# Performance work log

Measured on AMD Instinct MI355X. Metric: run time of the kernel, lower is better.

## Reference

```python
import jax, jax.numpy as jnp
import numpy as np

B, T, D, K = 16, 4096, 512, 256
ALPHA_MIN = 1e-6


def setup_inputs() -> dict:
    key = jax.random.key(0)
    ks = jax.random.split(key, 5)
    x = jax.random.normal(ks[0], (B, T, D), dtype=jnp.float32)
    # s_imag ~ U(-pi, pi) as in reset_parameters
    s_imag = jax.random.uniform(ks[1], (K,), minval=-np.pi, maxval=np.pi, dtype=jnp.float32)
    # s_real_raw = softplus^{-1}(target_alpha - alpha_min), target_alpha ~ U(0.01, 0.2)
    target_alpha = jax.random.uniform(ks[2], (K,), minval=0.01, maxval=0.2, dtype=jnp.float32)
    y = jnp.clip(target_alpha - ALPHA_MIN, 1e-8, None)
    s_real_raw = jnp.log(jnp.expm1(y))
    # projection weight/bias (spectral norm applied inside reference)
    W = jax.random.normal(ks[3], (K, D), dtype=jnp.float32) / np.sqrt(D)
    b = jnp.zeros((K,), dtype=jnp.float32)
    tau_raw = jnp.zeros((), dtype=jnp.float32)
    return {"x": x, "s_real_raw": s_real_raw, "s_imag": s_imag,
            "tau_raw": tau_raw, "W": W, "b": b}


def _spectral_normalize(W):
    # one power iteration from a fixed random u (mirrors torch spectral_norm buffer,
    # n_power_iterations=1, eps=1e-7); u,v are stop-gradiented like torch buffers.
    eps = 1e-7
    u0 = jax.random.normal(jax.random.key(42), (W.shape[0],), dtype=W.dtype)
    u0 = u0 / jnp.maximum(jnp.linalg.norm(u0), eps)
    v = W.T @ u0
    v = v / jnp.maximum(jnp.linalg.norm(v), eps)
    u = W @ v
    u = u / jnp.maximum(jnp.linalg.norm(u), eps)
    u = jax.lax.stop_gradient(u)
    v = jax.lax.stop_gradient(v)
    sigma = u @ (W @ v)
    return W / sigma


def reference(x, s_real_raw, s_imag, tau_raw, W, b):
    Bx, Tx, Dx = x.shape
    k = s_imag.shape[0]
    tau = jax.nn.softplus(tau_raw) + 1e-3
    alpha0 = (jax.nn.softplus(s_real_raw) + ALPHA_MIN) * tau  # [k]
    omega0 = s_imag * tau                                     # [k]
    # dt is None path: uniform normalized time step
    dt = jnp.asarray(1.0 / max(Tx - 1, 1), dtype=x.dtype)
    rho = jnp.exp(-alpha0 * dt)   # [k], time-invariant since dt is constant
    ct = jnp.cos(omega0 * dt)     # [k]
    st = jnp.sin(omega0 * dt)     # [k]
    # spectral-normalized linear drive u_t = W_sn x_t + b  -> [B,T,k]
    u = jnp.einsum('btd,kd->btk', x, _spectral_normalize(W)) + b

    def step(carry, u_t):
        c, s = carry  # each [B,k]
        c_new = rho * (c * ct - s * st) + u_t
        s_new = rho * (c * st + s * ct)
        return (c_new, s_new), (c_new, s_new)

    z0 = (jnp.zeros((Bx, k), x.dtype), jnp.zeros((Bx, k), x.dtype))
    _, (C, S) = jax.lax.scan(step, z0, jnp.swapaxes(u, 0, 1))  # [T,B,k] each
    C = jnp.swapaxes(C, 0, 1)
    S = jnp.swapaxes(S, 0, 1)
    return jnp.concatenate([C, S], axis=2)  # [B,T,2k]
```

## Files before the change

### kernel.cpp

```cpp
#include <hip/hip_runtime.h>

#define Bsz 16
#define Tsz 4096
#define Dsz 512
#define Ksz 256
#define Msz (Bsz * Tsz)
#define CHUNK 64
#define NCH (Tsz / CHUNK)

typedef __attribute__((ext_vector_type(8))) short short8;
typedef __attribute__((ext_vector_type(4))) float f32x4;
typedef __attribute__((ext_vector_type(4))) unsigned int u32x4;

__device__ __forceinline__ unsigned int rotl32(unsigned int x, int d) {
  return (x << d) | (x >> (32 - d));
}

__device__ void threefry_pair(unsigned int c0, unsigned int c1,
                              unsigned int& o0, unsigned int& o1) {
  const unsigned int k0 = 0u, k1 = 42u;
  const unsigned int k2 = k0 ^ k1 ^ 0x1BD11BDAu;
  unsigned int x0 = c0 + k0;
  unsigned int x1 = c1 + k1;
#define TF_ROUND(r) { x0 += x1; x1 = rotl32(x1, (r)); x1 ^= x0; }
  TF_ROUND(13) TF_ROUND(15) TF_ROUND(26) TF_ROUND(6)
  x0 += k1; x1 += k2 + 1u;
  TF_ROUND(17) TF_ROUND(29) TF_ROUND(16) TF_ROUND(24)
  x0 += k2; x1 += k0 + 2u;
  TF_ROUND(13) TF_ROUND(15) TF_ROUND(26) TF_ROUND(6)
  x0 += k0; x1 += k1 + 3u;
  TF_ROUND(17) TF_ROUND(29) TF_ROUND(16) TF_ROUND(24)
  x0 += k1; x1 += k2 + 4u;
  TF_ROUND(13) TF_ROUND(15) TF_ROUND(26) TF_ROUND(6)
  x0 += k2; x1 += k0 + 5u;
#undef TF_ROUND
  o0 = x0; o1 = x1;
}

__device__ float erfinv32(float x) {
  float w = -log1pf(-x * x);
  float p;
  if (w < 5.f) {
    w -= 2.5f;
    p = 2.81022636e-08f;
    p = fmaf(p, w, 3.43273939e-07f);
    p = fmaf(p, w, -3.5233877e-06f);
    p = fmaf(p, w, -4.39150654e-06f);
    p = fmaf(p, w, 0.00021858087f);
    p = fmaf(p, w, -0.00125372503f);
    p = fmaf(p, w, -0.00417768164f);
    p = fmaf(p, w, 0.246640727f);
    p = fmaf(p, w, 1.50140941f);
  } else {
    w = sqrtf(w) - 3.f;
    p = -0.000200214257f;
    p = fmaf(p, w, 0.000100950558f);
    p = fmaf(p, w, 0.00134934322f);
    p = fmaf(p, w, -0.00367342844f);
    p = fmaf(p, w, 0.00573950773f);
    p = fmaf(p, w, -0.0076224613f);
    p = fmaf(p, w, 0.00943887047f);
    p = fmaf(p, w, 1.00167406f);
    p = fmaf(p, w, 2.83297682f);
  }
  return p * x;
}

__device__ float bits_to_normal(unsigned int bits) {
  unsigned int fb = (bits >> 9) | 0x3f800000u;
  float f = __uint_as_float(fb) - 1.0f;
  const float lo = -0.99999994f;
  float u = f * 2.0f + lo;
  u = fmaxf(lo, u);
  return 1.41421356f * erfinv32(u);
}

__device__ float block_sum_512(float v, float* s_red) {
  #pragma unroll
  for (int o = 32; o > 0; o >>= 1) v += __shfl_down(v, o);
  const int lane = threadIdx.x & 63, wid = threadIdx.x >> 6;
  if (lane == 0) s_red[wid] = v;
  __syncthreads();
  float r = 0.f;
  #pragma unroll
  for (int i = 0; i < 8; ++i) r += s_red[i];
  __syncthreads();
  return r;
}

__device__ __forceinline__ unsigned int bf16rne(float f) {
  unsigned int u = __float_as_uint(f);
  return (u + 0x7FFFu + ((u >> 16) & 1u)) >> 16;
}

__device__ __forceinline__ void gld16(const float* g, float* l) {
  using gp = const __attribute__((address_space(1))) unsigned int*;
  using lp = __attribute__((address_space(3))) unsigned int*;
  __builtin_amdgcn_global_load_lds((gp)(const void*)g, (lp)(void*)l, 16, 0, 0);
}

__global__ __launch_bounds__(512) void prep1_kernel(
    const float* __restrict__ W, float* __restrict__ partial_v) {
  __shared__ float s_u0[Ksz];
  __shared__ float s_red[8];
  const int tid = threadIdx.x;
  if (tid < 128) {
    unsigned int y0, y1;
    threefry_pair((unsigned int)tid, (unsigned int)(tid + 128), y0, y1);
    s_u0[tid] = bits_to_normal(y0);
    s_u0[tid + 128] = bits_to_normal(y1);
  }
  __syncthreads();
  float val = (tid < Ksz) ? s_u0[tid] * s_u0[tid] : 0.f;
  float ss = block_sum_512(val, s_red);
  float inv = 1.f / fmaxf(sqrtf(ss), 1e-7f);

  const int k0 = blockIdx.x * 16;
  float acc = 0.f;
  #pragma unroll
  for (int kk = 0; kk < 16; ++kk)
    acc = fmaf(W[(size_t)(k0 + kk) * Dsz + tid], s_u0[k0 + kk], acc);
  partial_v[blockIdx.x * Dsz + tid] = acc * inv;
}

__global__ __launch_bounds__(512) void prep2_kernel(
    const float* __restrict__ W, const float* __restrict__ partial_v,
    float* __restrict__ wv) {
  __shared__ float s_v[Dsz];
  __shared__ float s_red[8];
  __shared__ float s_p[8];
  const int tid = threadIdx.x;
  float acc = 0.f;
  #pragma unroll
  for (int b = 0; b < 16; ++b) acc += partial_v[b * Dsz + tid];
  float ssv = block_sum_512(acc * acc, s_red);
  float invv = 1.f / fmaxf(sqrtf(ssv), 1e-7f);
  s_v[tid] = acc * invv;
  __syncthreads();

  const int k = blockIdx.x * 4 + (tid >> 7);
  const int sub = tid & 127;
  const float* wr = W + (size_t)k * Dsz;
  float p = 0.f;
  #pragma unroll
  for (int j = sub; j < Dsz; j += 128) p = fmaf(wr[j], s_v[j], p);
  #pragma unroll
  for (int o = 32; o > 0; o >>= 1) p += __shfl_down(p, o);
  const int lane = tid & 63, wid = tid >> 6;
  if (lane == 0) s_p[wid] = p;
  __syncthreads();
  if (tid < 4) wv[blockIdx.x * 4 + tid] = s_p[2 * tid] + s_p[2 * tid + 1];
}

__global__ __launch_bounds__(256) void prep3_kernel(
    const float* __restrict__ s_real_raw, const float* __restrict__ s_imag,
    const float* __restrict__ tau_raw, const float* __restrict__ wv,
    float* __restrict__ consts) {
  __shared__ float s_p[4];
  const int tid = threadIdx.x;
  float v = wv[tid];
  float v2 = v * v;
  #pragma unroll
  for (int o = 32; o > 0; o >>= 1) v2 += __shfl_down(v2, o);
  const int lane = tid & 63, wid = tid >> 6;
  if (lane == 0) s_p[wid] = v2;
  __syncthreads();
  float sswv = s_p[0] + s_p[1] + s_p[2] + s_p[3];
  float sigma = sswv / fmaxf(sqrtf(sswv), 1e-7f);
  if (tid == 0) consts[12 * Ksz] = 1.f / sigma;

  float tr = tau_raw[0];
  float tau = fmaxf(tr, 0.f) + log1pf(expf(-fabsf(tr))) + 1e-3f;
  float srr = s_real_raw[tid];
  float sp = fmaxf(srr, 0.f) + log1pf(expf(-fabsf(srr)));
  float alpha0 = (sp + 1e-6f) * tau;
  float omega0 = s_imag[tid] * tau;
  const float dt = 1.f / 4095.f;
  float ad = alpha0 * dt, an = omega0 * dt;
  consts[tid]            = expf(-ad) * cosf(an);
  consts[Ksz + tid]      = expf(-ad) * sinf(an);
  consts[2 * Ksz + tid]  = expf(-ad * 64.f) * cosf(an * 64.f);
  consts[3 * Ksz + tid]  = expf(-ad * 64.f) * sinf(an * 64.f);
  consts[4 * Ksz + tid]  = expf(-ad * 4.f) * cosf(an * 4.f);
  consts[5 * Ksz + tid]  = expf(-ad * 4.f) * sinf(an * 4.f);
  consts[6 * Ksz + tid]  = expf(-ad * 8.f) * cosf(an * 8.f);
  consts[7 * Ksz + tid]  = expf(-ad * 8.f) * sinf(an * 8.f);
  consts[8 * Ksz + tid]  = expf(-ad * 16.f) * cosf(an * 16.f);
  consts[9 * Ksz + tid]  = expf(-ad * 16.f) * sinf(an * 16.f);
  consts[10 * Ksz + tid] = expf(-ad * 32.f) * cosf(an * 32.f);
  consts[11 * Ksz + tid] = expf(-ad * 32.f) * sinf(an * 32.f);
}

__global__ __launch_bounds__(64) void wpack_kernel(
    const float* __restrict__ W, const float* __restrict__ consts,
    unsigned int* __restrict__ WfH, unsigned int* __restrict__ WfL) {
  const int kb = blockIdx.x >> 4;
  const int nb = blockIdx.x & 15;
  const int lane = threadIdx.x;
  const int lr = lane & 15, lg = lane >> 4;
  const float inv_sigma = consts[12 * Ksz];
  const float* src = W + (size_t)(nb * 16 + lr) * Dsz + kb * 32 + lg * 8;
  float v[8];
  *(float4*)&v[0] = *(const float4*)src;
  *(float4*)&v[4] = *(const float4*)(src + 4);
  unsigned int hh[4], ll[4];
  #pragma unroll
  for (int i = 0; i < 4; ++i) {
    float v0 = v[2 * i] * inv_sigma, v1 = v[2 * i + 1] * inv_sigma;
    unsigned int u0 = __float_as_uint(v0);
    unsigned int u1 = __float_as_uint(v1);
    hh[i] = (u0 >> 16) | (u1 & 0xFFFF0000u);
    float r0 = v0 - __uint_as_float(u0 & 0xFFFF0000u);
    float r1 = v1 - __uint_as_float(u1 & 0xFFFF0000u);
    ll[i] = bf16rne(r0) | (bf16rne(r1) << 16);
  }
  const size_t off = (size_t)blockIdx.x * 256 + lane * 4;
  *(int4*)(WfH + off) = *(int4*)hh;
  *(int4*)(WfL + off) = *(int4*)ll;
}

__global__ __launch_bounds__(512, 2) void gemm_mfma(
    const float* __restrict__ X, const unsigned int* __restrict__ WfH,
    const unsigned int* __restrict__ WfL, const float* __restrict__ bias,
    const float* __restrict__ consts, unsigned short* __restrict__ U,
    float* __restrict__ carry) {
  __shared__ float ldsA[4][4096];

  const int tid = threadIdx.x;
  const size_t m0 = (size_t)blockIdx.x * 128;
  const int lane = tid & 63;
  const int wid = tid >> 6;
  const int wm = wid >> 2;
  const int wn = wid & 3;
  const int lr = lane & 15;
  const int lg = lane >> 4;

  const int srow = tid >> 3;
  const int scol = ((tid & 7) ^ (srow & 7)) * 4;
  const float* gs0 = X + (m0 + srow) * Dsz + scol;
  const float* gs1 = X + (m0 + 64 + srow) * Dsz + scol;

  #define STAGE(kb) do {                                                     \
    float* lb = &ldsA[(kb) & 3][0] + wid * 256;       \
    gld16(gs0 + (kb) * 32, lb);                                              \
    gld16(gs1 + (kb) * 32, lb + 2048);                                       \
  } while (0)

  const char* const wfhp = (const char*)WfH + (size_t)(wn * 4) * 1024 + lane * 16;
  const char* const wflp = (const char*)WfL + (size_t)(wn * 4) * 1024 + lane * 16;

  short8 bh[4], bl[4];
  #define LOADB(kb) do {                                                     \
    const size_t tb = (size_t)(kb) * 16384;                                  \
    _Pragma("unroll")                                                        \
    for (int q = 0; q < 4; ++q) {                                            \
      bh[q] = *(const short8*)(wfhp + tb + (size_t)q * 1024);                \
      bl[q] = *(const short8*)(wflp + tb + (size_t)q * 1024);                \
    }                                                                        \
  } while (0)

  f32x4 acc[4][4];
  #pragma unroll
  for (int i = 0; i < 4; ++i)
    #pragma unroll
    for (int j = 0; j < 4; ++j) acc[i][j] = (f32x4)(0.f);

  #define PAIR(slotp, p) do {                                                \
    short8 ah[2], al[2];                                                     \
    _Pragma("unroll")                                                        \
    for (int m = 0; m < 2; ++m) {                                            \
      const int R = wm * 64 + (2 * (p) + m) * 16 + lr;                       \
      const float* rb = (slotp) + R * 32;                                    \
      float4 va = *(const float4*)(rb + ((lg * 2) ^ (lr & 7)) * 4);          \
      float4 vb = *(const float4*)(rb + ((lg * 2 + 1) ^ (lr & 7)) * 4);      \
      float v[8] = {va.x, va.y, va.z, va.w, vb.x, vb.y, vb.z, vb.w};         \
      unsigned int hh[4], llw[4];                                            \
      _Pragma("unroll")                                                      \
      for (int i = 0; i < 4; ++i) {                                          \
        float v0 = v[2 * i], v1 = v[2 * i + 1];                              \
        unsigned int u0 = __float_as_uint(v0);                               \
        unsigned int u1 = __float_as_uint(v1);                               \
        hh[i] = (u0 >> 16) | (u1 & 0xFFFF0000u);                             \
        float r0 = v0 - __uint_as_float(u0 & 0xFFFF0000u);                   \
        float r1 = v1 - __uint_as_float(u1 & 0xFFFF0000u);                   \
        llw[i] = bf16rne(r0) | (bf16rne(r1) << 16);                          \
      }                                                                      \
      u32x4 th = {hh[0], hh[1], hh[2], hh[3]};                               \
      u32x4 tl = {llw[0], llw[1], llw[2], llw[3]};                           \
      ah[m] = __builtin_bit_cast(short8, th);                                \
      al[m] = __builtin_bit_cast(short8, tl);                                \
    }                                                                        \
    _Pragma("unroll")                                                        \
    for (int m = 0; m < 2; ++m)                                              \
      _Pragma("unroll")                                                      \
      for (int nf = 0; nf < 4; ++nf)                                         \
        acc[2 * (p) + m][nf] = __builtin_amdgcn_mfma_f32_16x16x32_bf16(      \
            ah[m], bh[nf], acc[2 * (p) + m][nf], 0, 0, 0);                   \
    _Pragma("unroll")                                                        \
    for (int m = 0; m < 2; ++m)                                              \
      _Pragma("unroll")                                                      \
      for (int nf = 0; nf < 4; ++nf)                                         \
        acc[2 * (p) + m][nf] = __builtin_amdgcn_mfma_f32_16x16x32_bf16(      \
            ah[m], bl[nf], acc[2 * (p) + m][nf], 0, 0, 0);                   \
    _Pragma("unroll")                                                        \
    for (int m = 0; m < 2; ++m)                                              \
      _Pragma("unroll")                                                      \
      for (int nf = 0; nf < 4; ++nf)                                         \
        acc[2 * (p) + m][nf] = __builtin_amdgcn_mfma_f32_16x16x32_bf16(      \
            al[m], bh[nf], acc[2 * (p) + m][nf], 0, 0, 0);                   \
  } while (0)

  STAGE(0);
  STAGE(1);

  for (int k = 0; k < 14; ++k) {
    LOADB(k);
    __builtin_amdgcn_sched_barrier(0);
    STAGE(k + 2);
    asm volatile("s_waitcnt vmcnt(2)" ::: "memory");
    __builtin_amdgcn_s_barrier();
    __builtin_amdgcn_sched_barrier(0);
    const float* slotp = &ldsA[k & 3][0];
    PAIR(slotp, 0);
    PAIR(slotp, 1);
  }
  #pragma unroll
  for (int k = 14; k < 16; ++k) {
    LOADB(k);
    asm volatile("s_waitcnt vmcnt(0)" ::: "memory");
    __builtin_amdgcn_s_barrier();
    __builtin_amdgcn_sched_barrier(0);
    const float* slotp = &ldsA[k & 3][0];
    PAIR(slotp, 0);
    PAIR(slotp, 1);
  }
  #undef PAIR
  #undef LOADB
  #undef STAGE

  #pragma unroll
  for (int nf = 0; nf < 4; ++nf) {
    const int n = wn * 64 + nf * 16 + lr;
    const float bv = bias[n];
    const float ar_ = consts[n],           ai_ = consts[Ksz + n];
    const float p4r = consts[4 * Ksz + n], p4i = consts[5 * Ksz + n];
    const float p8r = consts[6 * Ksz + n], p8i = consts[7 * Ksz + n];
    const float p16r = consts[8 * Ksz + n], p16i = consts[9 * Ksz + n];
    const int e = 3 - lg;
    const float b1r = (e & 1) ? p4r : 1.f, b1i = (e & 1) ? p4i : 0.f;
    const float b2r = (e & 2) ? p8r : 1.f, b2i = (e & 2) ? p8i : 0.f;
    float wr = b1r * b2r - b1i * b2i;
    float wi = b1r * b2i + b1i * b2r;
    float Sr = 0.f, Si = 0.f;
    #pragma unroll
    for (int mf = 3; mf >= 0; --mf) {
      float vr = wr, vi = wi;
      #pragma unroll
      for (int j = 3; j >= 0; --j) {
        const float u = acc[mf][nf][j] + bv;
        U[(m0 + wm * 64 + mf * 16 + lg * 4 + j) * Ksz + n] =
            (unsigned short)bf16rne(u);
        Sr = fmaf(u, vr, Sr);
        Si = fmaf(u, vi, Si);
        if (j) {
          float t_ = vr * ar_ - vi * ai_;
          vi = vr * ai_ + vi * ar_;
          vr = t_;
        }
      }
      if (mf) {
        float t_ = wr * p16r - wi * p16i;
        wi = wr * p16i + wi * p16r;
        wr = t_;
      }
    }
    Sr += __shfl_xor(Sr, 16); Si += __shfl_xor(Si, 16);
    Sr += __shfl_xor(Sr, 32); Si += __shfl_xor(Si, 32);
    if (lg == 0)
      ((float2*)carry)[(size_t)(blockIdx.x * 2 + wm) * Ksz + n] =
          make_float2(Sr, Si);
  }
}

__global__ __launch_bounds__(64) void scan_prefix(
    const float* __restrict__ consts, const float* __restrict__ carry,
    float* __restrict__ prefix) {
  const int k = blockIdx.y * 64 + threadIdx.x;
  const int b = blockIdx.x;
  const float Ar = consts[2 * Ksz + k], Ai = consts[3 * Ksz + k];
  const float2* cp = (const float2*)carry;
  float2* pp = (float2*)prefix;
  float c = 0.f, s = 0.f;
  for (int m = 0; m < NCH; ++m) {
    const size_t idx = (size_t)(b * NCH + m) * Ksz + k;
    pp[idx] = make_float2(c, s);
    float2 L = cp[idx];
    float cn = fmaf(Ar, c, fmaf(-Ai, s, L.x));
    float sn = fmaf(Ai, c, fmaf(Ar, s, L.y));
    c = cn; s = sn;
  }
}

__global__ __launch_bounds__(256) void scan_final(
    const unsigned short* __restrict__ U, const float* __restrict__ consts,
    const float* __restrict__ prefix, float* __restrict__ out) {
  const int k = threadIdx.x;
  const int bm = blockIdx.x;
  const float ar = consts[k], ai = consts[Ksz + k];
  float2 w = ((const float2*)prefix)[(size_t)bm * Ksz + k];
  float c = w.x, s = w.y;
  const unsigned short* up = U + (size_t)bm * (CHUNK * Ksz) + k;
  float* op = out + (size_t)bm * (CHUNK * 2 * Ksz);
  #pragma unroll 4
  for (int t = 0; t < CHUNK; ++t) {
    float u = __uint_as_float((unsigned int)up[(size_t)t * Ksz] << 16);
    float cn = fmaf(ar, c, fmaf(-ai, s, u));
    s = fmaf(ai, c, ar * s);
    c = cn;
    op[(size_t)t * 2 * Ksz + k] = c;
    op[(size_t)t * 2 * Ksz + Ksz + k] = s;
  }
}

extern "C" void kernel_launch(void* const* d_in, const int* in_sizes, int n_in,
                              void* d_out, int out_size, void* d_ws, size_t ws_size,
                              hipStream_t stream) {
  const float* x    = (const float*)d_in[0];
  const float* srr  = (const float*)d_in[1];
  const float* sim  = (const float*)d_in[2];
  const float* traw = (const float*)d_in[3];
  const float* W    = (const float*)d_in[4];
  const float* bias = (const float*)d_in[5];
  float* out = (float*)d_out;

  float* wsf    = (float*)d_ws;
  float* consts = wsf;
  unsigned short* U = (unsigned short*)(wsf + 4096);
  float* carry  = wsf + 4096 + 8388608;
  float* prefix = carry + (size_t)2 * Bsz * NCH * Ksz;
  unsigned int* WfH = (unsigned int*)(prefix + (size_t)2 * Bsz * NCH * Ksz);
  unsigned int* WfL = WfH + 65536;
  float* partial_v  = (float*)(WfL + 65536);
  float* wv         = partial_v + 16 * Dsz;

  prep1_kernel<<<16, 512, 0, stream>>>(W, partial_v);
  prep2_kernel<<<64, 512, 0, stream>>>(W, partial_v, wv);
  prep3_kernel<<<1, 256, 0, stream>>>(srr, sim, traw, wv, consts);
  wpack_kernel<<<256, 64, 0, stream>>>(W, consts, WfH, WfL);
  gemm_mfma<<<Msz / 128, 512, 0, stream>>>(x, WfH, WfL, bias, consts, U, carry);
  scan_prefix<<<dim3(Bsz, Ksz / 64), 64, 0, stream>>>(consts, carry, prefix);
  scan_final<<<Bsz * NCH, Ksz, 0, stream>>>(U, consts, prefix, out);
}
```

Before: 132.7 us.

## Shrink GEMM block to 64 rows with per-wave private LDS staging and double-buffered B

The GEMM block shrinks from 512 threads covering 128 rows to 256 threads covering 64 rows. Each wave now stages its own private copy of the 64-row X tile in LDS, double-buffered, so the per-tile workgroup s_barrier is dropped and only per-wave vmcnt waits remain. The W fragments are double-buffered in registers so the next tile's B loads overlap the current MFMAs. In exchange, each block reads the X tile four times (once per wave) and the grid doubles, with more register pressure from the extra B buffers.

```diff
diff --git a/kernel.cpp b/kernel.cpp
--- a/kernel.cpp
+++ b/kernel.cpp
@@ -219,43 +219,41 @@
   *(int4*)(WfL + off) = *(int4*)ll;
 }
 
-__global__ __launch_bounds__(512, 2) void gemm_mfma(
+__global__ __launch_bounds__(256, 2) void gemm_mfma(
     const float* __restrict__ X, const unsigned int* __restrict__ WfH,
     const unsigned int* __restrict__ WfL, const float* __restrict__ bias,
     const float* __restrict__ consts, unsigned short* __restrict__ U,
     float* __restrict__ carry) {
-  __shared__ float ldsA[4][4096];
+  __shared__ float lds[4][2][2048];
 
   const int tid = threadIdx.x;
-  const size_t m0 = (size_t)blockIdx.x * 128;
+  const size_t m0 = (size_t)blockIdx.x * 64;
   const int lane = tid & 63;
-  const int wid = tid >> 6;
-  const int wm = wid >> 2;
-  const int wn = wid & 3;
+  const int wn = tid >> 6;
   const int lr = lane & 15;
   const int lg = lane >> 4;
 
-  const int srow = tid >> 3;
-  const int scol = ((tid & 7) ^ (srow & 7)) * 4;
-  const float* gs0 = X + (m0 + srow) * Dsz + scol;
-  const float* gs1 = X + (m0 + 64 + srow) * Dsz + scol;
+  const int srow = lane >> 3;
+  const int scb = (lane & 7) ^ (srow & 7);
+  const float* gsA = X + (m0 + srow) * Dsz + scb * 4;
 
   #define STAGE(kb) do {                                                     \
-    float* lb = &ldsA[(kb) & 3][0] + wid * 256;       \
-    gld16(gs0 + (kb) * 32, lb);                                              \
-    gld16(gs1 + (kb) * 32, lb + 2048);                                       \
+    float* lb = &lds[wn][(kb) & 1][0];                                       \
+    _Pragma("unroll")                                                        \
+    for (int i = 0; i < 8; ++i)                                              \
+      gld16(gsA + (size_t)(8 * i) * Dsz + (kb) * 32, lb + i * 256);          \
   } while (0)
 
-  const char* const wfhp = (const char*)WfH + (size_t)(wn * 4) * 1024 + lane * 16;
-  const char* const wflp = (const char*)WfL + (size_t)(wn * 4) * 1024 + lane * 16;
-
-  short8 bh[4], bl[4];
-  #define LOADB(kb) do {                                                     \
+  const char* const wfhp = (const char*)WfH + (size_t)wn * 4096 + lane * 16;
+  const char* const wflp = (const char*)WfL + (size_t)wn * 4096 + lane * 16;
+
+  short8 bhA[4], blA[4], bhB[4], blB[4];
+  #define LOADB(bh_, bl_, kb) do {                                           \
     const size_t tb = (size_t)(kb) * 16384;                                  \
     _Pragma("unroll")                                                        \
     for (int q = 0; q < 4; ++q) {                                            \
-      bh[q] = *(const short8*)(wfhp + tb + (size_t)q * 1024);                \
-      bl[q] = *(const short8*)(wflp + tb + (size_t)q * 1024);                \
+      bh_[q] = *(const short8*)(wfhp + tb + (size_t)q * 1024);               \
+      bl_[q] = *(const short8*)(wflp + tb + (size_t)q * 1024);               \
     }                                                                        \
   } while (0)
 
@@ -265,11 +263,11 @@
     #pragma unroll
     for (int j = 0; j < 4; ++j) acc[i][j] = (f32x4)(0.f);
 
-  #define PAIR(slotp, p) do {                                                \
+  #define PAIR(slotp, p, bh_, bl_) do {                                      \
     short8 ah[2], al[2];                                                     \
     _Pragma("unroll")                                                        \
     for (int m = 0; m < 2; ++m) {                                            \
-      const int R = wm * 64 + (2 * (p) + m) * 16 + lr;                       \
+      const int R = (2 * (p) + m) * 16 + lr;                                 \
       const float* rb = (slotp) + R * 32;                                    \
       float4 va = *(const float4*)(rb + ((lg * 2) ^ (lr & 7)) * 4);          \
       float4 vb = *(const float4*)(rb + ((lg * 2 + 1) ^ (lr & 7)) * 4);      \
@@ -295,45 +293,46 @@
       _Pragma("unroll")                                                      \
       for (int nf = 0; nf < 4; ++nf)                                         \
         acc[2 * (p) + m][nf] = __builtin_amdgcn_mfma_f32_16x16x32_bf16(      \
-            ah[m], bh[nf], acc[2 * (p) + m][nf], 0, 0, 0);                   \
+            ah[m], bh_[nf], acc[2 * (p) + m][nf], 0, 0, 0);                  \
     _Pragma("unroll")                                                        \
     for (int m = 0; m < 2; ++m)                                              \
       _Pragma("unroll")                                                      \
       for (int nf = 0; nf < 4; ++nf)                                         \
         acc[2 * (p) + m][nf] = __builtin_amdgcn_mfma_f32_16x16x32_bf16(      \
-            ah[m], bl[nf], acc[2 * (p) + m][nf], 0, 0, 0);                   \
+            ah[m], bl_[nf], acc[2 * (p) + m][nf], 0, 0, 0);                  \
     _Pragma("unroll")                                                        \
     for (int m = 0; m < 2; ++m)                                              \
       _Pragma("unroll")                                                      \
       for (int nf = 0; nf < 4; ++nf)                                         \
         acc[2 * (p) + m][nf] = __builtin_amdgcn_mfma_f32_16x16x32_bf16(      \
-            al[m], bh[nf], acc[2 * (p) + m][nf], 0, 0, 0);                   \
+            al[m], bh_[nf], acc[2 * (p) + m][nf], 0, 0, 0);                  \
   } while (0)
 
-  STAGE(0);
-  STAGE(1);
-
-  for (int k = 0; k < 14; ++k) {
-    LOADB(k);
-    __builtin_amdgcn_sched_barrier(0);
-    STAGE(k + 2);
-    asm volatile("s_waitcnt vmcnt(2)" ::: "memory");
-    __builtin_amdgcn_s_barrier();
-    __builtin_amdgcn_sched_barrier(0);
-    const float* slotp = &ldsA[k & 3][0];
-    PAIR(slotp, 0);
-    PAIR(slotp, 1);
-  }
-  #pragma unroll
-  for (int k = 14; k < 16; ++k) {
-    LOADB(k);
-    asm volatile("s_waitcnt vmcnt(0)" ::: "memory");
-    __builtin_amdgcn_s_barrier();
-    __builtin_amdgcn_sched_barrier(0);
-    const float* slotp = &ldsA[k & 3][0];
-    PAIR(slotp, 0);
-    PAIR(slotp, 1);
-  }
+  #define SB() __builtin_amdgcn_sched_barrier(0)
+
+  #define TILE(k, bCh, bCl, bNh, bNl) do {                                   \
+    if ((k) + 1 < 16) {                                                      \
+      LOADB(bNh, bNl, (k) + 1); SB();                                        \
+      STAGE((k) + 1); SB();                                                  \
+      asm volatile("s_waitcnt vmcnt(16)" ::: "memory");                      \
+    } else {                                                                 \
+      asm volatile("s_waitcnt vmcnt(0)" ::: "memory");                       \
+    }                                                                        \
+    SB();                                                                    \
+    const float* slotp = &lds[wn][(k) & 1][0];                               \
+    PAIR(slotp, 0, bCh, bCl);                                                \
+    PAIR(slotp, 1, bCh, bCl);                                                \
+  } while (0)
+
+  LOADB(bhA, blA, 0); SB();
+  STAGE(0); SB();
+
+  for (int k = 0; k < 16; k += 2) {
+    TILE(k,     bhA, blA, bhB, blB);
+    TILE(k + 1, bhB, blB, bhA, blA);
+  }
+  #undef TILE
+  #undef SB
   #undef PAIR
   #undef LOADB
   #undef STAGE
@@ -358,8 +357,7 @@
       #pragma unroll
       for (int j = 3; j >= 0; --j) {
         const float u = acc[mf][nf][j] + bv;
-        U[(m0 + wm * 64 + mf * 16 + lg * 4 + j) * Ksz + n] =
-            (unsigned short)bf16rne(u);
+        U[(m0 + mf * 16 + lg * 4 + j) * Ksz + n] = (unsigned short)bf16rne(u);
         Sr = fmaf(u, vr, Sr);
         Si = fmaf(u, vi, Si);
         if (j) {
@@ -377,8 +375,7 @@
     Sr += __shfl_xor(Sr, 16); Si += __shfl_xor(Si, 16);
     Sr += __shfl_xor(Sr, 32); Si += __shfl_xor(Si, 32);
     if (lg == 0)
-      ((float2*)carry)[(size_t)(blockIdx.x * 2 + wm) * Ksz + n] =
-          make_float2(Sr, Si);
+      ((float2*)carry)[(size_t)blockIdx.x * Ksz + n] = make_float2(Sr, Si);
   }
 }
 
@@ -447,7 +444,7 @@
   prep2_kernel<<<64, 512, 0, stream>>>(W, partial_v, wv);
   prep3_kernel<<<1, 256, 0, stream>>>(srr, sim, traw, wv, consts);
   wpack_kernel<<<256, 64, 0, stream>>>(W, consts, WfH, WfL);
-  gemm_mfma<<<Msz / 128, 512, 0, stream>>>(x, WfH, WfL, bias, consts, U, carry);
+  gemm_mfma<<<Msz / 64, 256, 0, stream>>>(x, WfH, WfL, bias, consts, U, carry);
   scan_prefix<<<dim3(Bsz, Ksz / 64), 64, 0, stream>>>(consts, carry, prefix);
   scan_final<<<Bsz * NCH, Ksz, 0, stream>>>(U, consts, prefix, out);
 }
```

New measurement: 128.8 us. -2.9%, faster.
